# Optimization experiments

Hardware: AMD Instinct MI355X
Metric: run time of the kernel (lower is better)

The kernel has to match this reference:

```python
import jax, jax.numpy as jnp
import numpy as np

B, S, D, H = 4, 2048, 1024, 16
DK = D // H


def setup_inputs() -> dict:
    key = jax.random.key(0)
    ks = jax.random.split(key, 12)
    def xavier(k, shape):
        fan_in, fan_out = shape[1], shape[0]
        limit = (6.0 / (fan_in + fan_out)) ** 0.5
        return jax.random.uniform(k, shape, jnp.float32, -limit, limit)
    inp = {
        "q": jax.random.normal(ks[0], (B, S, D), jnp.float32),
        "k": jax.random.normal(ks[1], (B, S, D), jnp.float32),
        "v": jax.random.normal(ks[2], (B, S, D), jnp.float32),
        "mask": jnp.ones((1, 1, S, S), jnp.int32),
        "Wq": xavier(ks[3], (D, D)), "bq": jnp.zeros((D,), jnp.float32),
        "Wk": xavier(ks[4], (D, D)), "bk": jnp.zeros((D,), jnp.float32),
        "Wv": xavier(ks[5], (D, D)), "bv": jnp.zeros((D,), jnp.float32),
        "Wo": xavier(ks[6], (D, D)), "bo": jnp.zeros((D,), jnp.float32),
        "ln_g": jnp.ones((D,), jnp.float32),
        "ln_b": jnp.zeros((D,), jnp.float32),
    }
    return inp


def _split_heads(x):
    b, s, _ = x.shape
    return x.reshape(b, s, H, DK).transpose(0, 2, 1, 3)  # [B,H,S,dk]


def reference(q, k, v, mask, Wq, bq, Wk, bk, Wv, bv, Wo, bo, ln_g, ln_b):
    residual = q
    qh = _split_heads(q @ Wq.T + bq)
    kh = _split_heads(k @ Wk.T + bk)
    vh = _split_heads(v @ Wv.T + bv)
    scale = jnp.sqrt(jnp.asarray(DK, qh.dtype))
    scores = jnp.einsum("bhqd,bhkd->bhqk", qh, kh) / scale  # [B,H,S,S]
    scores = jnp.where(mask == 0, jnp.asarray(-1e9, scores.dtype), scores)
    m = jnp.max(scores, axis=-1, keepdims=True)
    e = jnp.exp(scores - m) * mask.astype(scores.dtype)
    probs = e / (jnp.sum(e, axis=-1, keepdims=True) + 1e-9)
    attn = jnp.einsum("bhqk,bhkd->bhqd", probs, vh)
    attn = attn.transpose(0, 2, 1, 3).reshape(q.shape[0], -1, D)
    out = attn @ Wo.T + bo
    x = out + residual
    mu = jnp.mean(x, axis=-1, keepdims=True)
    var = jnp.mean((x - mu) ** 2, axis=-1, keepdims=True)
    return (x - mu) / jnp.sqrt(var + 1e-5) * ln_g + ln_b
```

## Files before the change

### kernel.cpp

```cpp
#include <hip/hip_runtime.h>
#include <hip/hip_bf16.h>
#include <stdint.h>

#define B_  4
#define S_  2048
#define D_  1024
#define H_  16
#define DK_ 64
#define M_  (B_ * S_)

typedef __bf16 bf16x8 __attribute__((ext_vector_type(8)));
typedef float  f32x4  __attribute__((ext_vector_type(4)));

__device__ __forceinline__ void gl_lds16(const void* g, void* l) {
  __builtin_amdgcn_global_load_lds(
      (const __attribute__((address_space(1))) void*)g,
      (__attribute__((address_space(3))) void*)l, 16, 0, 0);
}

__device__ __forceinline__ bf16x8 pack8(float4 a, float4 b) {
  bf16x8 o;
  o[0] = (__bf16)a.x; o[1] = (__bf16)a.y; o[2] = (__bf16)a.z; o[3] = (__bf16)a.w;
  o[4] = (__bf16)b.x; o[5] = (__bf16)b.y; o[6] = (__bf16)b.z; o[7] = (__bf16)b.w;
  return o;
}

__global__ __launch_bounds__(256)
void cvt_w_kernel(const float* __restrict__ s0, const float* __restrict__ s1,
                  const float* __restrict__ s2, const float* __restrict__ s3,
                  __bf16* __restrict__ dst) {
  const float* s = blockIdx.y == 0 ? s0 : blockIdx.y == 1 ? s1
                  : blockIdx.y == 2 ? s2 : s3;
  __bf16* d = dst + (long)blockIdx.y * (D_ * D_);
  const int i = blockIdx.x * 256 + threadIdx.x;
  ((bf16x8*)d)[i] =
      pack8(((const float4*)s)[i * 2], ((const float4*)s)[i * 2 + 1]);
}

__global__ __launch_bounds__(256)
void cvt_x_kernel(const float* __restrict__ s0, const float* __restrict__ s1,
                  const float* __restrict__ s2, __bf16* __restrict__ d0,
                  __bf16* __restrict__ d1, __bf16* __restrict__ d2) {
  const float* s = blockIdx.y == 0 ? s0 : blockIdx.y == 1 ? s1 : s2;
  __bf16* d = blockIdx.y == 0 ? d0 : blockIdx.y == 1 ? d1 : d2;
  const int i = blockIdx.x * 256 + threadIdx.x;
  ((bf16x8*)d)[i] =
      pack8(((const float4*)s)[i * 2], ((const float4*)s)[i * 2 + 1]);
}

__global__ __launch_bounds__(256)
void proj_qkv_kernel(const __bf16* __restrict__ qb, const __bf16* __restrict__ kb,
                     const __bf16* __restrict__ vb, const __bf16* __restrict__ Wb,
                     const float* __restrict__ bq, const float* __restrict__ bk,
                     const float* __restrict__ bv, __bf16* __restrict__ Qh,
                     float qscale) {
  __shared__ __bf16 Asm[2][128 * 32];
  __shared__ __bf16 Bsm[2][128 * 32];
  const int lid  = blockIdx.x;
  const int slot = lid >> 3;
  const int G    = ((slot >> 3) << 3) + (lid & 7);
  const int z    = G >> 6;
  const int m0   = (G & 63) * 128;
  const int n0   = (slot & 7) * 128;

  const __bf16* A = z == 0 ? qb : z == 1 ? kb : vb;
  const __bf16* W = Wb + (long)z * (D_ * D_);
  const float* bias = z == 0 ? bq : z == 1 ? bk : bv;
  const float scale = z == 0 ? qscale : 1.0f;
  __bf16* dst = Qh + (long)z * ((long)M_ * D_);

  const int tid  = threadIdx.x;
  const int lane = tid & 63;
  const int wave = tid >> 6;
  const int wm = (wave >> 1) * 64, wn = (wave & 1) * 64;
  const int lr = lane & 15, lq = lane >> 4;

  const int r0 = tid >> 2;
  const int cg = ((tid & 3) ^ ((r0 >> 1) & 3)) * 8;
  const __bf16* Ap0 = A + (long)(m0 + r0) * D_ + cg;
  const __bf16* Ap1 = A + (long)(m0 + 64 + r0) * D_ + cg;
  const __bf16* Wp0 = W + (long)(n0 + r0) * D_ + cg;
  const __bf16* Wp1 = W + (long)(n0 + 64 + r0) * D_ + cg;

  int aoff[4], boff[4];
#pragma unroll
  for (int i = 0; i < 4; i++) {
    const int row = wm + i * 16 + lr;
    aoff[i] = row * 32 + ((lq ^ ((row >> 1) & 3)) * 8);
  }
#pragma unroll
  for (int j = 0; j < 4; j++) {
    const int row = wn + j * 16 + lr;
    boff[j] = row * 32 + ((lq ^ ((row >> 1) & 3)) * 8);
  }

  f32x4 acc[4][4] = {};

  gl_lds16(Ap0, &Asm[0][tid * 8]);
  gl_lds16(Ap1, &Asm[0][(256 + tid) * 8]);
  gl_lds16(Wp0, &Bsm[0][tid * 8]);
  gl_lds16(Wp1, &Bsm[0][(256 + tid) * 8]);
  __syncthreads();

  for (int t = 0; t < 31; t++) {
    const int cur = t & 1, nxt = cur ^ 1;
    const int k1 = (t + 1) * 32;
    gl_lds16(Ap0 + k1, &Asm[nxt][tid * 8]);
    gl_lds16(Ap1 + k1, &Asm[nxt][(256 + tid) * 8]);
    gl_lds16(Wp0 + k1, &Bsm[nxt][tid * 8]);
    gl_lds16(Wp1 + k1, &Bsm[nxt][(256 + tid) * 8]);
    bf16x8 af[4], bf[4];
#pragma unroll
    for (int i = 0; i < 4; i++) af[i] = *(const bf16x8*)&Asm[cur][aoff[i]];
#pragma unroll
    for (int j = 0; j < 4; j++) bf[j] = *(const bf16x8*)&Bsm[cur][boff[j]];
#pragma unroll
    for (int i = 0; i < 4; i++)
#pragma unroll
      for (int j = 0; j < 4; j++)
        acc[i][j] = __builtin_amdgcn_mfma_f32_16x16x32_bf16(af[i], bf[j],
                                                            acc[i][j], 0, 0, 0);
    __syncthreads();
  }
  {
    bf16x8 af[4], bf[4];
#pragma unroll
    for (int i = 0; i < 4; i++) af[i] = *(const bf16x8*)&Asm[1][aoff[i]];
#pragma unroll
    for (int j = 0; j < 4; j++) bf[j] = *(const bf16x8*)&Bsm[1][boff[j]];
#pragma unroll
    for (int i = 0; i < 4; i++)
#pragma unroll
      for (int j = 0; j < 4; j++)
        acc[i][j] = __builtin_amdgcn_mfma_f32_16x16x32_bf16(af[i], bf[j],
                                                            acc[i][j], 0, 0, 0);
  }

#pragma unroll
  for (int j = 0; j < 4; j++) {
    const int n = n0 + wn + j * 16 + lr;
    const float bb = bias[n];
#pragma unroll
    for (int i = 0; i < 4; i++) {
      const int mbase = m0 + wm + i * 16 + lq * 4;
#pragma unroll
      for (int r = 0; r < 4; r++) {
        const int m = mbase + r;
        const float v = (acc[i][j][r] + bb) * scale;
        const int b = m >> 11, s = m & (S_ - 1);
        const int h = n >> 6, dk = n & 63;
        dst[(((long)(b * H_ + h) * S_ + s)) * DK_ + dk] = (__bf16)v;
      }
    }
  }
}

__global__ __launch_bounds__(256)
void gemm_out_kernel(const __bf16* __restrict__ A, const __bf16* __restrict__ W,
                     const float* __restrict__ bias, float* __restrict__ outf,
                     const float* __restrict__ resid) {
  __shared__ __bf16 Asm[2][128 * 32];
  __shared__ __bf16 Bsm[2][128 * 32];
  const int lid  = blockIdx.x;
  const int slot = lid >> 3;
  const int G    = ((slot >> 3) << 3) + (lid & 7);
  const int m0   = G * 128;
  const int n0   = (slot & 7) * 128;

  const int tid  = threadIdx.x;
  const int lane = tid & 63;
  const int wave = tid >> 6;
  const int wm = (wave >> 1) * 64, wn = (wave & 1) * 64;
  const int lr = lane & 15, lq = lane >> 4;

  const int r0 = tid >> 2;
  const int cg = ((tid & 3) ^ ((r0 >> 1) & 3)) * 8;
  const __bf16* Ap0 = A + (long)(m0 + r0) * D_ + cg;
  const __bf16* Ap1 = A + (long)(m0 + 64 + r0) * D_ + cg;
  const __bf16* Wp0 = W + (long)(n0 + r0) * D_ + cg;
  const __bf16* Wp1 = W + (long)(n0 + 64 + r0) * D_ + cg;

  int aoff[4], boff[4];
#pragma unroll
  for (int i = 0; i < 4; i++) {
    const int row = wm + i * 16 + lr;
    aoff[i] = row * 32 + ((lq ^ ((row >> 1) & 3)) * 8);
  }
#pragma unroll
  for (int j = 0; j < 4; j++) {
    const int row = wn + j * 16 + lr;
    boff[j] = row * 32 + ((lq ^ ((row >> 1) & 3)) * 8);
  }

  f32x4 acc[4][4] = {};

  gl_lds16(Ap0, &Asm[0][tid * 8]);
  gl_lds16(Ap1, &Asm[0][(256 + tid) * 8]);
  gl_lds16(Wp0, &Bsm[0][tid * 8]);
  gl_lds16(Wp1, &Bsm[0][(256 + tid) * 8]);
  __syncthreads();

  for (int t = 0; t < 31; t++) {
    const int cur = t & 1, nxt = cur ^ 1;
    const int k1 = (t + 1) * 32;
    gl_lds16(Ap0 + k1, &Asm[nxt][tid * 8]);
    gl_lds16(Ap1 + k1, &Asm[nxt][(256 + tid) * 8]);
    gl_lds16(Wp0 + k1, &Bsm[nxt][tid * 8]);
    gl_lds16(Wp1 + k1, &Bsm[nxt][(256 + tid) * 8]);
    bf16x8 af[4], bf[4];
#pragma unroll
    for (int i = 0; i < 4; i++) af[i] = *(const bf16x8*)&Asm[cur][aoff[i]];
#pragma unroll
    for (int j = 0; j < 4; j++) bf[j] = *(const bf16x8*)&Bsm[cur][boff[j]];
#pragma unroll
    for (int i = 0; i < 4; i++)
#pragma unroll
      for (int j = 0; j < 4; j++)
        acc[i][j] = __builtin_amdgcn_mfma_f32_16x16x32_bf16(af[i], bf[j],
                                                            acc[i][j], 0, 0, 0);
    __syncthreads();
  }
  {
    bf16x8 af[4], bf[4];
#pragma unroll
    for (int i = 0; i < 4; i++) af[i] = *(const bf16x8*)&Asm[1][aoff[i]];
#pragma unroll
    for (int j = 0; j < 4; j++) bf[j] = *(const bf16x8*)&Bsm[1][boff[j]];
#pragma unroll
    for (int i = 0; i < 4; i++)
#pragma unroll
      for (int j = 0; j < 4; j++)
        acc[i][j] = __builtin_amdgcn_mfma_f32_16x16x32_bf16(af[i], bf[j],
                                                            acc[i][j], 0, 0, 0);
  }

#pragma unroll
  for (int j = 0; j < 4; j++) {
    const int n = n0 + wn + j * 16 + lr;
    const float bb = bias[n];
#pragma unroll
    for (int i = 0; i < 4; i++) {
      const int mbase = m0 + wm + i * 16 + lq * 4;
#pragma unroll
      for (int r = 0; r < 4; r++) {
        const int m = mbase + r;
        outf[(long)m * D_ + n] = acc[i][j][r] + bb + resid[(long)m * D_ + n];
      }
    }
  }
}

__global__ __launch_bounds__(256)
void transpose_v_kernel(const __bf16* __restrict__ Vh, __bf16* __restrict__ Vt) {
  __shared__ __bf16 tile[64 * 80];
  const int tid = threadIdx.x;
  const int bh = blockIdx.y;
  const int s0 = blockIdx.x * 64;
#pragma unroll
  for (int c = 0; c < 2; c++) {
    const int idx = c * 256 + tid;
    const int sl = idx >> 3, ch = idx & 7;
    *(uint4*)&tile[sl * 80 + ch * 8] =
        *(const uint4*)&Vh[((long)bh * S_ + s0 + sl) * DK_ + ch * 8];
  }
  __syncthreads();
#pragma unroll
  for (int c = 0; c < 2; c++) {
    const int idx = c * 256 + tid;
    const int dk = idx >> 3, ch = idx & 7;
    __bf16 tmp[8];
#pragma unroll
    for (int j = 0; j < 8; j++) tmp[j] = tile[(ch * 8 + j) * 80 + dk];
    *(uint4*)&Vt[((long)bh * DK_ + dk) * S_ + s0 + ch * 8] = *(const uint4*)tmp;
  }
}

__global__ __launch_bounds__(256)
void attn_kernel(const __bf16* __restrict__ Qh,
                 const __bf16* __restrict__ Kh,
                 const __bf16* __restrict__ Vt,
                 __bf16* __restrict__ ctx) {
  __shared__ __bf16 Ksm[2][64 * 64];
  __shared__ __bf16 Vsm[2][64 * 64];
  __shared__ __bf16 Psm[4 * 32 * 72];
  const int tid = threadIdx.x, lane = tid & 63, wave = tid >> 6;
  const int lr = lane & 15, lq = lane >> 4;
  const int lid = blockIdx.x;
  const int slot = lid >> 3;
  const int bh = (lid & 7) * 8 + (slot >> 4);
  const int q0 = (slot & 15) * 128 + wave * 32;
  const long base = (long)bh * S_ * DK_;
  __bf16* Pw = &Psm[wave * 32 * 72];

  bf16x8 qf[2][2];
#pragma unroll
  for (int qg = 0; qg < 2; qg++)
#pragma unroll
    for (int c = 0; c < 2; c++)
      qf[qg][c] = *(const bf16x8*)
          &Qh[base + (long)(q0 + qg * 16 + lr) * DK_ + c * 32 + lq * 8];

  const int cl0 = (lq ^ (lr & 7)) * 8;
  const int cl1 = ((lq + 4) ^ (lr & 7)) * 8;
  const int rbase = lr * 64;

  const int row0 = tid >> 3;
  const int cg0  = ((tid & 7) ^ (row0 & 7)) * 8;
  const int row1 = (256 + tid) >> 3;
  const int cg1  = ((tid & 7) ^ (row1 & 7)) * 8;
  const __bf16* Kp0 = &Kh[base + (long)row0 * DK_ + cg0];
  const __bf16* Kp1 = &Kh[base + (long)row1 * DK_ + cg1];
  const __bf16* Vp0 = &Vt[base + (long)row0 * S_ + cg0];
  const __bf16* Vp1 = &Vt[base + (long)row1 * S_ + cg1];

  f32x4 o[2][4] = {};
  float lsum[2] = {0.f, 0.f};

#define STAGE_KV(kt_, b_)                                         \
  do {                                                            \
    const int koff_ = (kt_) * 64;                                 \
    gl_lds16(Kp0 + (long)koff_ * DK_, &Ksm[b_][tid * 8]);         \
    gl_lds16(Kp1 + (long)koff_ * DK_, &Ksm[b_][(256 + tid) * 8]); \
    gl_lds16(Vp0 + koff_, &Vsm[b_][tid * 8]);                     \
    gl_lds16(Vp1 + koff_, &Vsm[b_][(256 + tid) * 8]);             \
  } while (0)

  STAGE_KV(0, 0);
  __syncthreads();

#pragma unroll 2
  for (int kt = 0; kt < S_ / 64; kt++) {
    const int cur = kt & 1;
    if (kt < S_ / 64 - 1) STAGE_KV(kt + 1, cur ^ 1);
    const __bf16* Kc = Ksm[cur];
    const __bf16* Vc = Vsm[cur];

    f32x4 sc[2][4];
#pragma unroll
    for (int nt = 0; nt < 4; nt++) {
      bf16x8 kf0 = *(const bf16x8*)&Kc[nt * 1024 + rbase + cl0];
      bf16x8 kf1 = *(const bf16x8*)&Kc[nt * 1024 + rbase + cl1];
#pragma unroll
      for (int qg = 0; qg < 2; qg++) {
        f32x4 z = {};
        z = __builtin_amdgcn_mfma_f32_16x16x32_bf16(kf0, qf[qg][0], z, 0, 0, 0);
        z = __builtin_amdgcn_mfma_f32_16x16x32_bf16(kf1, qf[qg][1], z, 0, 0, 0);
        sc[qg][nt] = z;
      }
    }

#pragma unroll
    for (int qg = 0; qg < 2; qg++) {
      float rs = 0.f;
      __bf16* prow = &Pw[(qg * 16 + lr) * 72 + lq * 4];
#pragma unroll
      for (int nt = 0; nt < 4; nt++) {
        union { __bf16 h[4]; uint2 u; } pk;
#pragma unroll
        for (int r = 0; r < 4; r++) {
          const float p = __builtin_amdgcn_exp2f(sc[qg][nt][r]);
          rs += p;
          pk.h[r] = (__bf16)p;
        }
        *(uint2*)&prow[nt * 16] = pk.u;
      }
      lsum[qg] += rs;
    }

    bf16x8 pf[2][2];
#pragma unroll
    for (int qg = 0; qg < 2; qg++) {
      pf[qg][0] = *(const bf16x8*)&Pw[(qg * 16 + lr) * 72 + lq * 8];
      pf[qg][1] = *(const bf16x8*)&Pw[(qg * 16 + lr) * 72 + 32 + lq * 8];
    }
#pragma unroll
    for (int d = 0; d < 4; d++) {
      bf16x8 vf0 = *(const bf16x8*)&Vc[d * 1024 + rbase + cl0];
      bf16x8 vf1 = *(const bf16x8*)&Vc[d * 1024 + rbase + cl1];
#pragma unroll
      for (int qg = 0; qg < 2; qg++) {
        o[qg][d] = __builtin_amdgcn_mfma_f32_16x16x32_bf16(pf[qg][0], vf0,
                                                           o[qg][d], 0, 0, 0);
        o[qg][d] = __builtin_amdgcn_mfma_f32_16x16x32_bf16(pf[qg][1], vf1,
                                                           o[qg][d], 0, 0, 0);
      }
    }
    __syncthreads();
  }
#undef STAGE_KV

  const int b = bh >> 4, h = bh & 15;
#pragma unroll
  for (int qg = 0; qg < 2; qg++) {
    float t = lsum[qg];
    t += __shfl_xor(t, 16);
    t += __shfl_xor(t, 32);
#pragma unroll
    for (int r = 0; r < 4; r++) {
      const float ls = __shfl(t, (lane & 48) | (lq * 4 + r));
      const float inv = 1.f / (ls + 1e-9f);
      const int srow = q0 + qg * 16 + lq * 4 + r;
#pragma unroll
      for (int d = 0; d < 4; d++)
        ctx[((long)b * S_ + srow) * D_ + h * DK_ + d * 16 + lr] =
            (__bf16)(o[qg][d][r] * inv);
    }
  }
}

__global__ __launch_bounds__(256)
void ln_kernel(float* __restrict__ x, const float* __restrict__ g,
               const float* __restrict__ bta) {
  const int lane = threadIdx.x & 63, wave = threadIdx.x >> 6;
  const int row = blockIdx.x * 4 + wave;
  float* xp = x + (long)row * D_;
  float v[16], sum = 0.f, ssq = 0.f;
#pragma unroll
  for (int c = 0; c < 4; c++) {
    const float4 t = *(const float4*)&xp[lane * 16 + c * 4];
    v[c * 4 + 0] = t.x; v[c * 4 + 1] = t.y; v[c * 4 + 2] = t.z; v[c * 4 + 3] = t.w;
  }
#pragma unroll
  for (int j = 0; j < 16; j++) {
    sum += v[j];
    ssq += v[j] * v[j];
  }
#pragma unroll
  for (int off = 1; off < 64; off <<= 1) {
    sum += __shfl_xor(sum, off);
    ssq += __shfl_xor(ssq, off);
  }
  const float mu = sum * (1.f / 1024.f);
  const float var = ssq * (1.f / 1024.f) - mu * mu;
  const float rstd = rsqrtf(var + 1e-5f);
#pragma unroll
  for (int c = 0; c < 4; c++) {
    float4 t;
    const int cbase = lane * 16 + c * 4;
    t.x = (v[c * 4 + 0] - mu) * rstd * g[cbase + 0] + bta[cbase + 0];
    t.y = (v[c * 4 + 1] - mu) * rstd * g[cbase + 1] + bta[cbase + 1];
    t.z = (v[c * 4 + 2] - mu) * rstd * g[cbase + 2] + bta[cbase + 2];
    t.w = (v[c * 4 + 3] - mu) * rstd * g[cbase + 3] + bta[cbase + 3];
    *(float4*)&xp[cbase] = t;
  }
}

extern "C" void kernel_launch(void* const* d_in, const int* in_sizes, int n_in,
                              void* d_out, int out_size, void* d_ws,
                              size_t ws_size, hipStream_t stream) {
  const float* q   = (const float*)d_in[0];
  const float* k   = (const float*)d_in[1];
  const float* v   = (const float*)d_in[2];
  const float* Wq  = (const float*)d_in[4];
  const float* bq  = (const float*)d_in[5];
  const float* Wk  = (const float*)d_in[6];
  const float* bk  = (const float*)d_in[7];
  const float* Wv  = (const float*)d_in[8];
  const float* bv  = (const float*)d_in[9];
  const float* Wo  = (const float*)d_in[10];
  const float* bo  = (const float*)d_in[11];
  const float* lng = (const float*)d_in[12];
  const float* lnb = (const float*)d_in[13];
  float* out = (float*)d_out;
  __bf16* ws = (__bf16*)d_ws;

  const long SZ = (long)M_ * D_;
  const long WN = (long)D_ * D_;
  __bf16* Wb  = ws;
  __bf16* Qh  = ws + 4 * WN;
  __bf16* Kh  = Qh + SZ;
  __bf16* Vh  = Qh + 2 * SZ;
  __bf16* Vt  = Qh + 3 * SZ;
  __bf16* ctx = Vh;

  __bf16* qb = (__bf16*)out;
  __bf16* kb = qb + SZ;
  __bf16* vb = Vt;

  const float qscale = 0.125f * 1.44269504f;

  cvt_w_kernel<<<dim3(WN / 8 / 256, 4), 256, 0, stream>>>(Wq, Wk, Wv, Wo, Wb);
  cvt_x_kernel<<<dim3(SZ / 8 / 256, 3), 256, 0, stream>>>(q, k, v, qb, kb, vb);
  proj_qkv_kernel<<<1536, 256, 0, stream>>>(qb, kb, vb, Wb, bq, bk, bv, Qh,
                                            qscale);
  transpose_v_kernel<<<dim3(S_ / 64, B_ * H_), 256, 0, stream>>>(Vh, Vt);
  attn_kernel<<<1024, 256, 0, stream>>>(Qh, Kh, Vt, ctx);
  gemm_out_kernel<<<512, 256, 0, stream>>>(ctx, Wb + 3 * WN, bo, out, q);
  ln_kernel<<<M_ / 4, 256, 0, stream>>>(out, lng, lnb);
}
```

Measured before the change: 402.8 us.

## Switch attention to 32x32x16 MFMA and keep P in registers via permlane32_swap

Rewrites the attention inner loop to use 32x32x16 bf16 MFMAs with transposed operand roles, so the score tile lands in a layout where the exp'd probabilities can be rearranged with permlane32_swap and fed straight into the PV MFMA. This removes the per-wave LDS round trip for P (shared-memory write, read and its buffer). It also simplifies the row-sum reduction and the output store. The risk is the correctness of the lane mapping and a change in register pressure from the larger accumulators.

```diff
diff --git a/kernel.cpp b/kernel.cpp
--- a/kernel.cpp
+++ b/kernel.cpp
@@ -11,6 +11,7 @@
 
 typedef __bf16 bf16x8 __attribute__((ext_vector_type(8)));
 typedef float  f32x4  __attribute__((ext_vector_type(4)));
+typedef float  f32x16 __attribute__((ext_vector_type(16)));
 
 __device__ __forceinline__ void gl_lds16(const void* g, void* l) {
   __builtin_amdgcn_global_load_lds(
@@ -282,27 +283,21 @@
                  __bf16* __restrict__ ctx) {
   __shared__ __bf16 Ksm[2][64 * 64];
   __shared__ __bf16 Vsm[2][64 * 64];
-  __shared__ __bf16 Psm[4 * 32 * 72];
   const int tid = threadIdx.x, lane = tid & 63, wave = tid >> 6;
-  const int lr = lane & 15, lq = lane >> 4;
+  const int l31 = lane & 31;
+  const int h   = lane >> 5;
   const int lid = blockIdx.x;
   const int slot = lid >> 3;
   const int bh = (lid & 7) * 8 + (slot >> 4);
   const int q0 = (slot & 15) * 128 + wave * 32;
   const long base = (long)bh * S_ * DK_;
-  __bf16* Pw = &Psm[wave * 32 * 72];
-
-  bf16x8 qf[2][2];
-#pragma unroll
-  for (int qg = 0; qg < 2; qg++)
-#pragma unroll
-    for (int c = 0; c < 2; c++)
-      qf[qg][c] = *(const bf16x8*)
-          &Qh[base + (long)(q0 + qg * 16 + lr) * DK_ + c * 32 + lq * 8];
-
-  const int cl0 = (lq ^ (lr & 7)) * 8;
-  const int cl1 = ((lq + 4) ^ (lr & 7)) * 8;
-  const int rbase = lr * 64;
+
+  bf16x8 qf[4];
+#pragma unroll
+  for (int s = 0; s < 4; s++)
+    qf[s] = *(const bf16x8*)&Qh[base + (long)(q0 + l31) * DK_ + s * 16 + h * 8];
+
+  const int xorv = (l31 & 7) * 8;
 
   const int row0 = tid >> 3;
   const int cg0  = ((tid & 7) ^ (row0 & 7)) * 8;
@@ -313,8 +308,8 @@
   const __bf16* Vp0 = &Vt[base + (long)row0 * S_ + cg0];
   const __bf16* Vp1 = &Vt[base + (long)row1 * S_ + cg1];
 
-  f32x4 o[2][4] = {};
-  float lsum[2] = {0.f, 0.f};
+  f32x16 o0 = {}, o1 = {};
+  float lsum = 0.f;
 
 #define STAGE_KV(kt_, b_)                                         \
   do {                                                            \
@@ -335,76 +330,74 @@
     const __bf16* Kc = Ksm[cur];
     const __bf16* Vc = Vsm[cur];
 
-    f32x4 sc[2][4];
-#pragma unroll
-    for (int nt = 0; nt < 4; nt++) {
-      bf16x8 kf0 = *(const bf16x8*)&Kc[nt * 1024 + rbase + cl0];
-      bf16x8 kf1 = *(const bf16x8*)&Kc[nt * 1024 + rbase + cl1];
-#pragma unroll
-      for (int qg = 0; qg < 2; qg++) {
-        f32x4 z = {};
-        z = __builtin_amdgcn_mfma_f32_16x16x32_bf16(kf0, qf[qg][0], z, 0, 0, 0);
-        z = __builtin_amdgcn_mfma_f32_16x16x32_bf16(kf1, qf[qg][1], z, 0, 0, 0);
-        sc[qg][nt] = z;
+    f32x16 z0 = {}, z1 = {};
+#pragma unroll
+    for (int s = 0; s < 4; s++) {
+      const int ch = 2 * s + h;
+      bf16x8 kf0 = *(const bf16x8*)&Kc[l31 * 64 + ((ch * 8) ^ xorv)];
+      bf16x8 kf1 = *(const bf16x8*)&Kc[(32 + l31) * 64 + ((ch * 8) ^ xorv)];
+      z0 = __builtin_amdgcn_mfma_f32_32x32x16_bf16(kf0, qf[s], z0, 0, 0, 0);
+      z1 = __builtin_amdgcn_mfma_f32_32x32x16_bf16(kf1, qf[s], z1, 0, 0, 0);
+    }
+
+    uint32_t Dw[2][4][2];
+#pragma unroll
+    for (int kb = 0; kb < 2; kb++) {
+      const f32x16& z = kb ? z1 : z0;
+#pragma unroll
+      for (int m = 0; m < 4; m++) {
+#pragma unroll
+        for (int w = 0; w < 2; w++) {
+          const float pa = __builtin_amdgcn_exp2f(z[m * 4 + 2 * w]);
+          const float pb = __builtin_amdgcn_exp2f(z[m * 4 + 2 * w + 1]);
+          lsum += pa + pb;
+          union { __bf16 b[2]; uint32_t u; } pk;
+          pk.b[0] = (__bf16)pa;
+          pk.b[1] = (__bf16)pb;
+          Dw[kb][m][w] = pk.u;
+        }
       }
     }
 
 #pragma unroll
-    for (int qg = 0; qg < 2; qg++) {
-      float rs = 0.f;
-      __bf16* prow = &Pw[(qg * 16 + lr) * 72 + lq * 4];
-#pragma unroll
-      for (int nt = 0; nt < 4; nt++) {
-        union { __bf16 h[4]; uint2 u; } pk;
-#pragma unroll
-        for (int r = 0; r < 4; r++) {
-          const float p = __builtin_amdgcn_exp2f(sc[qg][nt][r]);
-          rs += p;
-          pk.h[r] = (__bf16)p;
+    for (int kb = 0; kb < 2; kb++) {
+#pragma unroll
+      for (int t = 0; t < 2; t++) {
+        const auto r0s = __builtin_amdgcn_permlane32_swap(
+            Dw[kb][2 * t][0], Dw[kb][2 * t + 1][0], false, false);
+        const auto r1s = __builtin_amdgcn_permlane32_swap(
+            Dw[kb][2 * t][1], Dw[kb][2 * t + 1][1], false, false);
+        union { uint32_t u[4]; bf16x8 f; } pf;
+        pf.u[0] = r0s[0]; pf.u[1] = r1s[0]; pf.u[2] = r0s[1]; pf.u[3] = r1s[1];
+        const int chv = 4 * kb + 2 * t + h;
+        {
+          bf16x8 vf0 = *(const bf16x8*)&Vc[l31 * 64 + ((chv * 8) ^ xorv)];
+          o0 = __builtin_amdgcn_mfma_f32_32x32x16_bf16(vf0, pf.f, o0, 0, 0, 0);
+          bf16x8 vf1 = *(const bf16x8*)&Vc[(32 + l31) * 64 + ((chv * 8) ^ xorv)];
+          o1 = __builtin_amdgcn_mfma_f32_32x32x16_bf16(vf1, pf.f, o1, 0, 0, 0);
         }
-        *(uint2*)&prow[nt * 16] = pk.u;
-      }
-      lsum[qg] += rs;
-    }
-
-    bf16x8 pf[2][2];
-#pragma unroll
-    for (int qg = 0; qg < 2; qg++) {
-      pf[qg][0] = *(const bf16x8*)&Pw[(qg * 16 + lr) * 72 + lq * 8];
-      pf[qg][1] = *(const bf16x8*)&Pw[(qg * 16 + lr) * 72 + 32 + lq * 8];
-    }
-#pragma unroll
-    for (int d = 0; d < 4; d++) {
-      bf16x8 vf0 = *(const bf16x8*)&Vc[d * 1024 + rbase + cl0];
-      bf16x8 vf1 = *(const bf16x8*)&Vc[d * 1024 + rbase + cl1];
-#pragma unroll
-      for (int qg = 0; qg < 2; qg++) {
-        o[qg][d] = __builtin_amdgcn_mfma_f32_16x16x32_bf16(pf[qg][0], vf0,
-                                                           o[qg][d], 0, 0, 0);
-        o[qg][d] = __builtin_amdgcn_mfma_f32_16x16x32_bf16(pf[qg][1], vf1,
-                                                           o[qg][d], 0, 0, 0);
       }
     }
     __syncthreads();
   }
 #undef STAGE_KV
 
-  const int b = bh >> 4, h = bh & 15;
-#pragma unroll
-  for (int qg = 0; qg < 2; qg++) {
-    float t = lsum[qg];
-    t += __shfl_xor(t, 16);
-    t += __shfl_xor(t, 32);
-#pragma unroll
-    for (int r = 0; r < 4; r++) {
-      const float ls = __shfl(t, (lane & 48) | (lq * 4 + r));
-      const float inv = 1.f / (ls + 1e-9f);
-      const int srow = q0 + qg * 16 + lq * 4 + r;
-#pragma unroll
-      for (int d = 0; d < 4; d++)
-        ctx[((long)b * S_ + srow) * D_ + h * DK_ + d * 16 + lr] =
-            (__bf16)(o[qg][d][r] * inv);
-    }
+  const float tt = lsum + __shfl_xor(lsum, 32);
+  const float inv = 1.f / (tt + 1e-9f);
+  const int b = bh >> 4, hh = bh & 15;
+  const long crow = ((long)b * S_ + q0 + l31) * D_ + hh * DK_;
+#pragma unroll
+  for (int db = 0; db < 2; db++) {
+    const f32x16& o = db ? o1 : o0;
+#pragma unroll
+    for (int m = 0; m < 4; m++)
+#pragma unroll
+      for (int wp = 0; wp < 2; wp++) {
+        union { __bf16 bb[2]; uint32_t u; } pk;
+        pk.bb[0] = (__bf16)(o[m * 4 + 2 * wp] * inv);
+        pk.bb[1] = (__bf16)(o[m * 4 + 2 * wp + 1] * inv);
+        *(uint32_t*)&ctx[crow + db * 32 + m * 8 + h * 4 + wp * 2] = pk.u;
+      }
   }
 }
 
```

After: 388.7 us. 3.5% less time.
